# Optimization experiments

Hardware: AMD Instinct MI355X
Metric: run time of the kernel (lower is better)

## Reference

```python
import jax, jax.numpy as jnp
import numpy as np

LN_EPS = 1e-5

def _layer_norm(x, g, b):
    mu = jnp.mean(x, axis=-1, keepdims=True)
    var = jnp.mean(jnp.square(x - mu), axis=-1, keepdims=True)
    return g * (x - mu) * jax.lax.rsqrt(var + LN_EPS) + b

def setup_inputs() -> dict:
    key = jax.random.key(0)
    ks = jax.random.split(key, 12)
    N, E, D, V = 25000, 400000, 128, 16
    x = jax.random.normal(ks[0], (N, 3), dtype=jnp.float32)
    h = jax.random.normal(ks[1], (N, D), dtype=jnp.float32)
    edge_index = jax.random.randint(ks[2], (2, E), 0, N, dtype=jnp.int64)
    local_frames = jax.random.normal(ks[3], (N, 3, 3), dtype=jnp.float32)
    batch = jnp.zeros((N,), dtype=jnp.int64)
    v_prev = jax.random.normal(ks[4], (N, V, 3), dtype=jnp.float32)
    # vector_init params: Linear(D, 3V) -> LN -> SiLU -> Linear(3V, 3V) -> LN -> SiLU
    lim1 = np.sqrt(6.0 / (D + 3 * V))
    W1 = jax.random.uniform(ks[5], (3 * V, D), minval=-lim1, maxval=lim1, dtype=jnp.float32)
    b1 = jnp.zeros((3 * V,), jnp.float32)
    g1 = jnp.ones((3 * V,), jnp.float32); bb1 = jnp.zeros((3 * V,), jnp.float32)
    lim2 = np.sqrt(6.0 / (3 * V + 3 * V))
    W2 = jax.random.uniform(ks[6], (3 * V, 3 * V), minval=-lim2, maxval=lim2, dtype=jnp.float32)
    b2 = jnp.zeros((3 * V,), jnp.float32)
    g2 = jnp.ones((3 * V,), jnp.float32); bb2 = jnp.zeros((3 * V,), jnp.float32)
    # vector_interaction params: Linear(2D, 2V*V) -> LN -> Sigmoid
    limi = np.sqrt(6.0 / (2 * D + 2 * V * V))
    Wi = jax.random.uniform(ks[7], (2 * V * V, 2 * D), minval=-limi, maxval=limi, dtype=jnp.float32)
    bi = jnp.zeros((2 * V * V,), jnp.float32)
    gi = jnp.ones((2 * V * V,), jnp.float32); bbi = jnp.zeros((2 * V * V,), jnp.float32)
    return {"x": x, "h": h, "edge_index": edge_index, "local_frames": local_frames,
            "batch": batch, "v_prev": v_prev,
            "W1": W1, "b1": b1, "g1": g1, "bb1": bb1,
            "W2": W2, "b2": b2, "g2": g2, "bb2": bb2,
            "Wi": Wi, "bi": bi, "gi": gi, "bbi": bbi}

def reference(x, h, edge_index, local_frames, batch, v_prev,
              W1, b1, g1, bb1, W2, b2, g2, bb2, Wi, bi, gi, bbi):
    N = x.shape[0]
    V = v_prev.shape[1]  # vector_dim
    row, col = edge_index[0], edge_index[1]
    # vector_init: two Linear+LN+SiLU blocks -> [N, V, 3]
    t = jax.nn.silu(_layer_norm(h @ W1.T + b1, g1, bb1))
    t = jax.nn.silu(_layer_norm(t @ W2.T + b2, g2, bb2))
    vectors = t.reshape(N, V, 3)
    hi, hj = h[col], h[row]           # [E, D]
    vi, vj = vectors[col], vectors[row]  # [E, V, 3]
    Ri, Rj = local_frames[col], local_frames[row]  # [E, 3, 3]
    # R_rel = Ri^T @ Rj
    R_rel = jnp.einsum('eji,ejk->eik', Ri, Rj)
    vj_in_i = jnp.einsum('eij,ecj->eci', R_rel, vj)  # rotate sender vectors
    stacked_vectors = jnp.concatenate([vi, vj_in_i], axis=1)  # [E, 2V, 3]
    stacked_norms = jnp.concatenate([hi, hj], axis=-1)        # [E, 2D]
    w = jax.nn.sigmoid(_layer_norm(stacked_norms @ Wi.T + bi, gi, bbi))
    int_weights = w.reshape(-1, 2 * V, V)                     # [E, 2V, V]
    v_new = jnp.einsum('eko,ekc->eco', stacked_vectors, int_weights)  # [E, V, 3]
    v_out = jax.ops.segment_sum(v_new, col, num_segments=N)  # scatter-add on receiver
    return v_prev + v_out
```

## Files before the change

kernel.cpp:

```cpp
#include <hip/hip_runtime.h>


#define DD 128
#define VV 16
#define TV 48
#define NK 512

__device__ __forceinline__ float bf2f_hi(unsigned u){
    union{unsigned u; float f;} v; v.u = u & 0xffff0000u; return v.f;
}
__device__ __forceinline__ float bf2f_lo(unsigned u){
    union{unsigned u; float f;} v; v.u = u << 16; return v.f;
}
__device__ __forceinline__ unsigned short f2bf(float f){
    union{float f; unsigned u;} v; v.f = f;
    unsigned r = v.u + 0x7fffu + ((v.u >> 16) & 1u);
    return (unsigned short)(r >> 16);
}
__device__ __forceinline__ void unpack8(uint4 q, float* d){
    d[0]=bf2f_lo(q.x); d[1]=bf2f_hi(q.x);
    d[2]=bf2f_lo(q.y); d[3]=bf2f_hi(q.y);
    d[4]=bf2f_lo(q.z); d[5]=bf2f_hi(q.z);
    d[6]=bf2f_lo(q.w); d[7]=bf2f_hi(q.w);
}
__device__ __forceinline__ float waveRedSum64(float v){
    #pragma unroll
    for (int off = 32; off > 0; off >>= 1) v += __shfl_xor(v, off, 64);
    return v;
}

__global__ void detect_i64(const int* p, int nchk, int* flag){
    __shared__ int s;
    if (threadIdx.x == 0) s = 0;
    __syncthreads();
    int nz = 0;
    for (int i = threadIdx.x; i < nchk; i += blockDim.x) nz |= (p[2*i+1] != 0);
    if (nz) atomicOr(&s, 1);
    __syncthreads();
    if (threadIdx.x == 0) *flag = s ? 0 : 1;
}

__global__ void zero_cnt(int* cnt, int n){
    int i = blockIdx.x*blockDim.x + threadIdx.x;
    if (i < n) cnt[i] = 0;
}

__global__ void cvt_hist(const void* __restrict__ src, int* __restrict__ dst,
                         int* __restrict__ cnt, int n, int E,
                         const int* __restrict__ flag){
    int i = blockIdx.x*blockDim.x + threadIdx.x;
    if (i >= n) return;
    int v = (*flag) ? (int)((const long long*)src)[i] : ((const int*)src)[i];
    dst[i] = v;
    if (i >= E) atomicAdd(&cnt[v], 1);
}

__global__ __launch_bounds__(1024) void scan_k(const int* __restrict__ cnt,
        int* __restrict__ start, int* __restrict__ cursor, int N){
    __shared__ int wsum[16];
    __shared__ int woff[16];
    __shared__ int btot;
    __shared__ int carry;
    int tid = threadIdx.x;
    int lane = tid & 63, wid = tid >> 6;
    if (tid == 0) carry = 0;
    __syncthreads();
    for (int base = 0; base < N; base += 1024){
        int i = base + tid;
        int x = (i < N) ? cnt[i] : 0;
        int v = x;
        #pragma unroll
        for (int off = 1; off < 64; off <<= 1){
            int t = __shfl_up(v, off, 64);
            if (lane >= off) v += t;
        }
        if (lane == 63) wsum[wid] = v;
        __syncthreads();
        if (wid == 0 && lane < 16){
            int s = wsum[lane];
            int sv = s;
            #pragma unroll
            for (int off = 1; off < 16; off <<= 1){
                int t = __shfl_up(sv, off, 64);
                if (lane >= off) sv += t;
            }
            woff[lane] = sv - s;
            if (lane == 15) btot = sv;
        }
        __syncthreads();
        if (i < N){
            int excl = v - x + woff[wid] + carry;
            start[i] = excl;
            cursor[i] = excl;
        }
        __syncthreads();
        if (tid == 0) carry += btot;
        __syncthreads();
    }
    if (tid == 0) start[N] = carry;
}

__global__ void scatter_k(const int* __restrict__ idx, int* __restrict__ cursor,
                          int* __restrict__ elist, int E){
    int e = blockIdx.x*blockDim.x + threadIdx.x;
    if (e >= E) return;
    int col = idx[E + e], row = idx[e];
    int pos = atomicAdd(&cursor[col], 1);
    elist[pos] = row;
}

__global__ void build_wt(const float* __restrict__ Wi, const float* __restrict__ bi,
                         const float* __restrict__ gi, const float* __restrict__ bbi,
                         float* __restrict__ Wt, float* __restrict__ bias_t,
                         float* __restrict__ gi_t, float* __restrict__ bbi_t){
    int j = blockIdx.x;
    int d = threadIdx.x;
    int half = j >> 9;
    int jj = j & 511;
    int c = jj >> 5, kk = jj & 31;
    int k = kk*16 + c;
    Wt[d*1024 + j] = Wi[k*256 + half*128 + d];
    if (d == 0){
        bias_t[j] = half ? 0.0f : bi[k];
        if (!half){ gi_t[jj] = gi[k]; bbi_t[jj] = bbi[k]; }
    }
}

__global__ __launch_bounds__(256) void vinit(
        const float* __restrict__ h,
        const float* __restrict__ W1, const float* __restrict__ b1,
        const float* __restrict__ g1, const float* __restrict__ bb1,
        const float* __restrict__ W2, const float* __restrict__ b2,
        const float* __restrict__ g2, const float* __restrict__ bb2,
        const float* __restrict__ frames,
        float* __restrict__ vecs, float* __restrict__ gvec, int N){
    __shared__ float hs[4][DD];
    __shared__ float ts[4][TV];
    int w = threadIdx.x >> 6, l = threadIdx.x & 63;
    int n = blockIdx.x*4 + w;
    int nr = n < N ? n : N-1;
    hs[w][l]      = h[(size_t)nr*DD + l];
    hs[w][l + 64] = h[(size_t)nr*DD + 64 + l];
    __syncthreads();

    float o1 = 0.0f;
    if (l < TV){
        o1 = b1[l];
        const float* wr = W1 + l*DD;
        #pragma unroll
        for (int d = 0; d < DD; d += 4){
            float4 w4 = *(const float4*)(wr + d);
            o1 += hs[w][d]*w4.x + hs[w][d+1]*w4.y + hs[w][d+2]*w4.z + hs[w][d+3]*w4.w;
        }
    }
    float s  = waveRedSum64(l < TV ? o1 : 0.0f);
    float mu = s * (1.0f/TV);
    float dv = l < TV ? (o1 - mu) : 0.0f;
    float sq = waveRedSum64(dv*dv);
    float inv = rsqrtf(sq*(1.0f/TV) + 1e-5f);
    if (l < TV){
        float y = g1[l]*(dv*inv) + bb1[l];
        ts[w][l] = y / (1.0f + __expf(-y));
    }
    __syncthreads();

    float o2 = 0.0f;
    if (l < TV){
        o2 = b2[l];
        const float* wr = W2 + l*TV;
        #pragma unroll
        for (int j = 0; j < TV; j += 4){
            float4 w4 = *(const float4*)(wr + j);
            o2 += ts[w][j]*w4.x + ts[w][j+1]*w4.y + ts[w][j+2]*w4.z + ts[w][j+3]*w4.w;
        }
    }
    s  = waveRedSum64(l < TV ? o2 : 0.0f);
    mu = s * (1.0f/TV);
    dv = l < TV ? (o2 - mu) : 0.0f;
    sq = waveRedSum64(dv*dv);
    inv = rsqrtf(sq*(1.0f/TV) + 1e-5f);
    __syncthreads();
    if (l < TV){
        float y = g2[l]*(dv*inv) + bb2[l];
        float t2 = y / (1.0f + __expf(-y));
        if (n < N) vecs[(size_t)n*TV + l] = t2;
        ts[w][l] = t2;
    }
    __syncthreads();
    if (l < TV && n < N){
        int cc = l/3, oo = l%3;
        const float* R = frames + (size_t)n*9;
        float gv = R[oo*3+0]*ts[w][cc*3+0] + R[oo*3+1]*ts[w][cc*3+1] + R[oo*3+2]*ts[w][cc*3+2];
        gvec[(size_t)n*TV + l] = gv;
    }
}

#define BM 64
#define BN 128
#define BK 32
__global__ __launch_bounds__(256) void gemm_p(
        const float* __restrict__ h, const float* __restrict__ Wt,
        const float* __restrict__ bias_t, unsigned short* __restrict__ P, int N){
    __shared__ float As[BK][BM];
    __shared__ float Bs[BK][BN + 4];
    int tid = threadIdx.x;
    int n0 = blockIdx.x * BN;
    int m0 = blockIdx.y * BM;
    int tm = tid >> 4, tn = tid & 15;
    float acc[4][8];
    #pragma unroll
    for (int i = 0; i < 4; i++)
        #pragma unroll
        for (int j = 0; j < 8; j++) acc[i][j] = 0.0f;

    int lm  = tid >> 2;
    int lc4 = tid & 3;
    int grow = m0 + lm; if (grow > N-1) grow = N-1;
    const float* hp = h + (size_t)grow*DD + lc4*8;
    int bkb = tid >> 5;
    int bjj = tid & 31;

    for (int kt = 0; kt < DD; kt += BK){
        float4 a0 = *(const float4*)(hp + kt);
        float4 a1 = *(const float4*)(hp + kt + 4);
        As[lc4*8+0][lm] = a0.x; As[lc4*8+1][lm] = a0.y;
        As[lc4*8+2][lm] = a0.z; As[lc4*8+3][lm] = a0.w;
        As[lc4*8+4][lm] = a1.x; As[lc4*8+5][lm] = a1.y;
        As[lc4*8+6][lm] = a1.z; As[lc4*8+7][lm] = a1.w;
        #pragma unroll
        for (int r = 0; r < 4; r++){
            float4 b4 = *(const float4*)(Wt + (size_t)(kt + bkb*4 + r)*1024 + n0 + bjj*4);
            *(float4*)&Bs[bkb*4+r][bjj*4] = b4;
        }
        __syncthreads();
        #pragma unroll
        for (int k = 0; k < BK; k++){
            float4 a   = *(const float4*)&As[k][tm*4];
            float4 blo = *(const float4*)&Bs[k][tn*4];
            float4 bhi = *(const float4*)&Bs[k][64 + tn*4];
            float am[4] = {a.x, a.y, a.z, a.w};
            float bv[8] = {blo.x, blo.y, blo.z, blo.w, bhi.x, bhi.y, bhi.z, bhi.w};
            #pragma unroll
            for (int mi = 0; mi < 4; mi++)
                #pragma unroll
                for (int ni = 0; ni < 8; ni++)
                    acc[mi][ni] = fmaf(am[mi], bv[ni], acc[mi][ni]);
        }
        __syncthreads();
    }
    #pragma unroll
    for (int mi = 0; mi < 4; mi++){
        size_t rowm = (size_t)(m0 + tm*4 + mi);
        ushort4 olo, ohi;
        olo.x = f2bf(acc[mi][0] + bias_t[n0 + tn*4 + 0]);
        olo.y = f2bf(acc[mi][1] + bias_t[n0 + tn*4 + 1]);
        olo.z = f2bf(acc[mi][2] + bias_t[n0 + tn*4 + 2]);
        olo.w = f2bf(acc[mi][3] + bias_t[n0 + tn*4 + 3]);
        ohi.x = f2bf(acc[mi][4] + bias_t[n0 + 64 + tn*4 + 0]);
        ohi.y = f2bf(acc[mi][5] + bias_t[n0 + 64 + tn*4 + 1]);
        ohi.z = f2bf(acc[mi][6] + bias_t[n0 + 64 + tn*4 + 2]);
        ohi.w = f2bf(acc[mi][7] + bias_t[n0 + 64 + tn*4 + 3]);
        *(ushort4*)(P + rowm*1024 + n0 + tn*4)      = olo;
        *(ushort4*)(P + rowm*1024 + n0 + 64 + tn*4) = ohi;
    }
}

__global__ __launch_bounds__(256) void node_k(
        const unsigned short* __restrict__ P,
        const float* __restrict__ vecs, const float* __restrict__ gvec,
        const float* __restrict__ frames, const int* __restrict__ start,
        const int* __restrict__ elist, const float* __restrict__ vprev,
        const float* __restrict__ gi_t, const float* __restrict__ bbi_t,
        float* __restrict__ out, int N){
    __shared__ float vi_s[4][TV];
    __shared__ float vj_s[4][4][52];
    int wv = threadIdx.x >> 6, ln = threadIdx.x & 63;
    int sub = ln >> 4, c = ln & 15;
    int n0 = blockIdx.x*4 + wv;
    int n = n0 < N ? n0 : N-1;

    if (ln < TV) vi_s[wv][ln] = vecs[(size_t)n*TV + ln];
    float R[9];
    #pragma unroll
    for (int i = 0; i < 9; i++) R[i] = frames[(size_t)n*9 + i];

    float pa[32];
    {
        const uint4* p4 = (const uint4*)(P + (size_t)n*1024 + c*32);
        #pragma unroll
        for (int q = 0; q < 4; q++) unpack8(p4[q], pa + 8*q);
    }
    int e0 = start[n], e1 = start[n+1];
    float a0 = 0.f, a1 = 0.f, a2 = 0.f;

    for (int t = e0 + sub; t < e1; t += 4){
        int row = elist[t];
        float l[32]; float s = 0.f;
        {
            const uint4* p4 = (const uint4*)(P + (size_t)row*1024 + 512 + c*32);
            #pragma unroll
            for (int q = 0; q < 4; q++){
                float tmp[8]; unpack8(p4[q], tmp);
                #pragma unroll
                for (int r = 0; r < 8; r++){
                    float x = pa[8*q+r] + tmp[r];
                    l[8*q+r] = x; s += x;
                }
            }
        }
        #pragma unroll
        for (int off = 1; off < 16; off <<= 1) s += __shfl_xor(s, off, 64);
        float mu = s * (1.0f/NK);
        float sq = 0.f;
        #pragma unroll
        for (int i = 0; i < 32; i++){ float d = l[i] - mu; l[i] = d; sq = fmaf(d, d, sq); }
        #pragma unroll
        for (int off = 1; off < 16; off <<= 1) sq += __shfl_xor(sq, off, 64);
        float inv = rsqrtf(sq*(1.0f/NK) + 1e-5f);

        float w[32];
        {
            const float4* g4 = (const float4*)(gi_t  + c*32);
            const float4* b4 = (const float4*)(bbi_t + c*32);
            #pragma unroll
            for (int q = 0; q < 8; q++){
                float4 gg = g4[q], bb = b4[q];
                float gx[4] = {gg.x, gg.y, gg.z, gg.w};
                float bx[4] = {bb.x, bb.y, bb.z, bb.w};
                #pragma unroll
                for (int r = 0; r < 4; r++){
                    float y = fmaf(gx[r], l[4*q+r]*inv, bx[r]);
                    w[4*q+r] = 1.0f / (1.0f + __expf(-y));
                }
            }
        }
        {
            const float* gr = gvec + (size_t)row*TV + c*3;
            float g0 = gr[0], g1 = gr[1], g2 = gr[2];
            #pragma unroll
            for (int i = 0; i < 3; i++)
                vj_s[wv][sub][c*3+i] = R[0+i]*g0 + R[3+i]*g1 + R[6+i]*g2;
        }
        #pragma unroll
        for (int kk = 0; kk < 16; kk++){
            float wl = w[kk], wh = w[16+kk];
            a0 = fmaf(vi_s[wv][kk*3+0], wl, a0);
            a1 = fmaf(vi_s[wv][kk*3+1], wl, a1);
            a2 = fmaf(vi_s[wv][kk*3+2], wl, a2);
            a0 = fmaf(vj_s[wv][sub][kk*3+0], wh, a0);
            a1 = fmaf(vj_s[wv][sub][kk*3+1], wh, a1);
            a2 = fmaf(vj_s[wv][sub][kk*3+2], wh, a2);
        }
    }
    a0 += __shfl_xor(a0,16,64); a0 += __shfl_xor(a0,32,64);
    a1 += __shfl_xor(a1,16,64); a1 += __shfl_xor(a1,32,64);
    a2 += __shfl_xor(a2,16,64); a2 += __shfl_xor(a2,32,64);
    if (ln < 16 && n0 < N){
        size_t o = (size_t)n*TV + c*3;
        out[o+0] = vprev[o+0] + a0;
        out[o+1] = vprev[o+1] + a1;
        out[o+2] = vprev[o+2] + a2;
    }
}

extern "C" void kernel_launch(void* const* d_in, const int* in_sizes, int n_in,
                              void* d_out, int out_size, void* d_ws, size_t ws_size,
                              hipStream_t stream){
    const float* h      = (const float*)d_in[1];
    const void*  eidx   = d_in[2];
    const float* frames = (const float*)d_in[3];
    const float* vprev  = (const float*)d_in[5];
    const float* W1  = (const float*)d_in[6];
    const float* b1  = (const float*)d_in[7];
    const float* g1  = (const float*)d_in[8];
    const float* bb1 = (const float*)d_in[9];
    const float* W2  = (const float*)d_in[10];
    const float* b2  = (const float*)d_in[11];
    const float* g2  = (const float*)d_in[12];
    const float* bb2 = (const float*)d_in[13];
    const float* Wi  = (const float*)d_in[14];
    const float* bi  = (const float*)d_in[15];
    const float* gi  = (const float*)d_in[16];
    const float* bbi = (const float*)d_in[17];
    float* out = (float*)d_out;

    const int N = in_sizes[1] / DD;
    const int E = in_sizes[2] / 2;
    const int Np = ((N + 63) / 64) * 64;

    float* ws     = (float*)d_ws;
    float* Wt     = ws;
    float* bias_t = Wt + 131072;
    float* gi_t   = bias_t + 1024;
    float* bbi_t  = gi_t + 512;
    float* vecs   = bbi_t + 512;
    float* gvec   = vecs + (size_t)N*TV;
    unsigned short* P = (unsigned short*)(gvec + (size_t)N*TV);
    int*   idx32  = (int*)(P + (size_t)Np*1024);
    int*   cnt    = idx32 + 2*(size_t)E;
    int*   startp = cnt + N;
    int*   cursor = startp + N + 1;
    int*   elist  = cursor + N;
    int*   dflag  = elist + E;

    int nchk = E < 4096 ? E : 4096;
    detect_i64<<<1, 256, 0, stream>>>((const int*)eidx, nchk, dflag);
    zero_cnt<<<(N + 255)/256, 256, 0, stream>>>(cnt, N);
    cvt_hist<<<(2*E + 255)/256, 256, 0, stream>>>(eidx, idx32, cnt, 2*E, E, dflag);
    build_wt<<<1024, 128, 0, stream>>>(Wi, bi, gi, bbi, Wt, bias_t, gi_t, bbi_t);
    vinit<<<(N + 3)/4, 256, 0, stream>>>(h, W1, b1, g1, bb1, W2, b2, g2, bb2,
                                         frames, vecs, gvec, N);
    dim3 ggrid(1024/BN, Np/BM);
    gemm_p<<<ggrid, 256, 0, stream>>>(h, Wt, bias_t, P, N);
    scan_k<<<1, 1024, 0, stream>>>(cnt, startp, cursor, N);
    scatter_k<<<(E + 255)/256, 256, 0, stream>>>(idx32, cursor, elist, E);
    node_k<<<(N + 3)/4, 256, 0, stream>>>(P, vecs, gvec, frames, startp, elist,
                                          vprev, gi_t, bbi_t, out, N);
    (void)ws_size; (void)n_in; (void)out_size;
}
```

Measured before the change: 590.8 us.

## Use bf16 MFMA with hi/lo split for projection GEMM, store fp32 P

Replaces the scalar FP32 tiled GEMM with an MFMA bf16 kernel. The h operand is split into high and low bf16 parts to keep accuracy, while the weights are cast to bf16. The intermediate P is now stored as fp32 rather than bf16, which doubles gather traffic in node_k. node_k also switches to a single-pass mean/variance LayerNorm, folds the sign into gi/bbi, and precomputes rotated sender vectors into a shared buffer. This trades extra memory bandwidth in the edge loop for a much cheaper GEMM and less ALU work per edge.

```diff
diff --git a/kernel.cpp b/kernel.cpp
--- a/kernel.cpp
+++ b/kernel.cpp
@@ -6,27 +6,16 @@
 #define TV 48
 #define NK 512
 
-__device__ __forceinline__ float bf2f_hi(unsigned u){
-    union{unsigned u; float f;} v; v.u = u & 0xffff0000u; return v.f;
-}
-__device__ __forceinline__ float bf2f_lo(unsigned u){
-    union{unsigned u; float f;} v; v.u = u << 16; return v.f;
-}
+typedef __attribute__((ext_vector_type(8))) short short8;
+typedef __attribute__((ext_vector_type(4))) float f32x4;
+
 __device__ __forceinline__ unsigned short f2bf(float f){
     union{float f; unsigned u;} v; v.f = f;
     unsigned r = v.u + 0x7fffu + ((v.u >> 16) & 1u);
     return (unsigned short)(r >> 16);
 }
-__device__ __forceinline__ void unpack8(uint4 q, float* d){
-    d[0]=bf2f_lo(q.x); d[1]=bf2f_hi(q.x);
-    d[2]=bf2f_lo(q.y); d[3]=bf2f_hi(q.y);
-    d[4]=bf2f_lo(q.z); d[5]=bf2f_hi(q.z);
-    d[6]=bf2f_lo(q.w); d[7]=bf2f_hi(q.w);
-}
-__device__ __forceinline__ float waveRedSum64(float v){
-    #pragma unroll
-    for (int off = 32; off > 0; off >>= 1) v += __shfl_xor(v, off, 64);
-    return v;
+__device__ __forceinline__ float bf2f(unsigned short h){
+    union{unsigned u; float f;} v; v.u = ((unsigned)h) << 16; return v.f;
 }
 
 __global__ void detect_i64(const int* p, int nchk, int* flag){
@@ -111,7 +100,7 @@
 
 __global__ void build_wt(const float* __restrict__ Wi, const float* __restrict__ bi,
                          const float* __restrict__ gi, const float* __restrict__ bbi,
-                         float* __restrict__ Wt, float* __restrict__ bias_t,
+                         unsigned short* __restrict__ Wtb, float* __restrict__ bias_t,
                          float* __restrict__ gi_t, float* __restrict__ bbi_t){
     int j = blockIdx.x;
     int d = threadIdx.x;
@@ -119,13 +108,30 @@
     int jj = j & 511;
     int c = jj >> 5, kk = jj & 31;
     int k = kk*16 + c;
-    Wt[d*1024 + j] = Wi[k*256 + half*128 + d];
+    Wtb[(size_t)j*128 + d] = f2bf(Wi[k*256 + half*128 + d]);
     if (d == 0){
         bias_t[j] = half ? 0.0f : bi[k];
-        if (!half){ gi_t[jj] = gi[k]; bbi_t[jj] = bbi[k]; }
-    }
-}
-
+        if (!half){ gi_t[jj] = -gi[k]; bbi_t[jj] = -bbi[k]; }
+    }
+}
+
+__global__ void cast_h(const float* __restrict__ h, unsigned short* __restrict__ hbh,
+                       unsigned short* __restrict__ hbl, int N, int total){
+    int i = blockIdx.x*blockDim.x + threadIdx.x;
+    if (i >= total) return;
+    int m = i >> 7;
+    float v = (m < N) ? h[i] : 0.0f;
+    unsigned short hi = f2bf(v);
+    float lo = v - bf2f(hi);
+    hbh[i] = hi;
+    hbl[i] = f2bf(lo);
+}
+
+__device__ __forceinline__ float waveRedSum64(float v){
+    #pragma unroll
+    for (int off = 32; off > 0; off >>= 1) v += __shfl_xor(v, off, 64);
+    return v;
+}
 __global__ __launch_bounds__(256) void vinit(
         const float* __restrict__ h,
         const float* __restrict__ W1, const float* __restrict__ b1,
@@ -195,130 +201,118 @@
     }
 }
 
-#define BM 64
-#define BN 128
-#define BK 32
-__global__ __launch_bounds__(256) void gemm_p(
-        const float* __restrict__ h, const float* __restrict__ Wt,
-        const float* __restrict__ bias_t, unsigned short* __restrict__ P, int N){
-    __shared__ float As[BK][BM];
-    __shared__ float Bs[BK][BN + 4];
-    int tid = threadIdx.x;
-    int n0 = blockIdx.x * BN;
-    int m0 = blockIdx.y * BM;
-    int tm = tid >> 4, tn = tid & 15;
-    float acc[4][8];
+__global__ __launch_bounds__(256) void gemm_mfma(
+        const unsigned short* __restrict__ hbh, const unsigned short* __restrict__ hbl,
+        const unsigned short* __restrict__ Wtb, const float* __restrict__ bias_t,
+        float* __restrict__ P, int Np){
+    int wv = threadIdx.x >> 6, l = threadIdx.x & 63;
+    int lr = l & 15, g = l >> 4;
+    int m0 = (blockIdx.y*4 + wv)*16;
+    int n0 = blockIdx.x*256;
+
+    f32x4 acc[16];
     #pragma unroll
-    for (int i = 0; i < 4; i++)
-        #pragma unroll
-        for (int j = 0; j < 8; j++) acc[i][j] = 0.0f;
-
-    int lm  = tid >> 2;
-    int lc4 = tid & 3;
-    int grow = m0 + lm; if (grow > N-1) grow = N-1;
-    const float* hp = h + (size_t)grow*DD + lc4*8;
-    int bkb = tid >> 5;
-    int bjj = tid & 31;
-
-    for (int kt = 0; kt < DD; kt += BK){
-        float4 a0 = *(const float4*)(hp + kt);
-        float4 a1 = *(const float4*)(hp + kt + 4);
-        As[lc4*8+0][lm] = a0.x; As[lc4*8+1][lm] = a0.y;
-        As[lc4*8+2][lm] = a0.z; As[lc4*8+3][lm] = a0.w;
-        As[lc4*8+4][lm] = a1.x; As[lc4*8+5][lm] = a1.y;
-        As[lc4*8+6][lm] = a1.z; As[lc4*8+7][lm] = a1.w;
+    for (int nf = 0; nf < 16; nf++) acc[nf] = (f32x4){0.f,0.f,0.f,0.f};
+
+    const unsigned short* arow_h = hbh + (size_t)(m0 + lr)*128;
+    const unsigned short* arow_l = hbl + (size_t)(m0 + lr)*128;
+
+    #pragma unroll
+    for (int ks = 0; ks < 128; ks += 32){
+        int kb = ks + 4*g;
+        short8 ah, al;
+        ((ushort4*)&ah)[0] = *(const ushort4*)(arow_h + kb);
+        ((ushort4*)&ah)[1] = *(const ushort4*)(arow_h + kb + 16);
+        ((ushort4*)&al)[0] = *(const ushort4*)(arow_l + kb);
+        ((ushort4*)&al)[1] = *(const ushort4*)(arow_l + kb + 16);
+        #pragma unroll
+        for (int nf = 0; nf < 16; nf++){
+            const unsigned short* brow = Wtb + (size_t)(n0 + nf*16 + lr)*128;
+            short8 b;
+            ((ushort4*)&b)[0] = *(const ushort4*)(brow + kb);
+            ((ushort4*)&b)[1] = *(const ushort4*)(brow + kb + 16);
+            acc[nf] = __builtin_amdgcn_mfma_f32_16x16x32_bf16(ah, b, acc[nf], 0, 0, 0);
+            acc[nf] = __builtin_amdgcn_mfma_f32_16x16x32_bf16(al, b, acc[nf], 0, 0, 0);
+        }
+    }
+    #pragma unroll
+    for (int nf = 0; nf < 16; nf++){
+        int col = n0 + nf*16 + lr;
+        float bs = bias_t[col];
         #pragma unroll
         for (int r = 0; r < 4; r++){
-            float4 b4 = *(const float4*)(Wt + (size_t)(kt + bkb*4 + r)*1024 + n0 + bjj*4);
-            *(float4*)&Bs[bkb*4+r][bjj*4] = b4;
-        }
-        __syncthreads();
-        #pragma unroll
-        for (int k = 0; k < BK; k++){
-            float4 a   = *(const float4*)&As[k][tm*4];
-            float4 blo = *(const float4*)&Bs[k][tn*4];
-            float4 bhi = *(const float4*)&Bs[k][64 + tn*4];
-            float am[4] = {a.x, a.y, a.z, a.w};
-            float bv[8] = {blo.x, blo.y, blo.z, blo.w, bhi.x, bhi.y, bhi.z, bhi.w};
-            #pragma unroll
-            for (int mi = 0; mi < 4; mi++)
-                #pragma unroll
-                for (int ni = 0; ni < 8; ni++)
-                    acc[mi][ni] = fmaf(am[mi], bv[ni], acc[mi][ni]);
-        }
-        __syncthreads();
-    }
-    #pragma unroll
-    for (int mi = 0; mi < 4; mi++){
-        size_t rowm = (size_t)(m0 + tm*4 + mi);
-        ushort4 olo, ohi;
-        olo.x = f2bf(acc[mi][0] + bias_t[n0 + tn*4 + 0]);
-        olo.y = f2bf(acc[mi][1] + bias_t[n0 + tn*4 + 1]);
-        olo.z = f2bf(acc[mi][2] + bias_t[n0 + tn*4 + 2]);
-        olo.w = f2bf(acc[mi][3] + bias_t[n0 + tn*4 + 3]);
-        ohi.x = f2bf(acc[mi][4] + bias_t[n0 + 64 + tn*4 + 0]);
-        ohi.y = f2bf(acc[mi][5] + bias_t[n0 + 64 + tn*4 + 1]);
-        ohi.z = f2bf(acc[mi][6] + bias_t[n0 + 64 + tn*4 + 2]);
-        ohi.w = f2bf(acc[mi][7] + bias_t[n0 + 64 + tn*4 + 3]);
-        *(ushort4*)(P + rowm*1024 + n0 + tn*4)      = olo;
-        *(ushort4*)(P + rowm*1024 + n0 + 64 + tn*4) = ohi;
+            P[(size_t)(m0 + g*4 + r)*1024 + col] = acc[nf][r] + bs;
+        }
     }
 }
 
 __global__ __launch_bounds__(256) void node_k(
-        const unsigned short* __restrict__ P,
-        const float* __restrict__ vecs, const float* __restrict__ gvec,
-        const float* __restrict__ frames, const int* __restrict__ start,
-        const int* __restrict__ elist, const float* __restrict__ vprev,
-        const float* __restrict__ gi_t, const float* __restrict__ bbi_t,
-        float* __restrict__ out, int N){
-    __shared__ float vi_s[4][TV];
-    __shared__ float vj_s[4][4][52];
+        const float* __restrict__ P, const float* __restrict__ vecs,
+        const float* __restrict__ gvec, const float* __restrict__ frames,
+        const int* __restrict__ start, const int* __restrict__ elist,
+        const float* __restrict__ vprev, const float* __restrict__ gi_t,
+        const float* __restrict__ bbi_t, float* __restrict__ out, int N){
+    __shared__ float svs[4][4][100];
     int wv = threadIdx.x >> 6, ln = threadIdx.x & 63;
     int sub = ln >> 4, c = ln & 15;
     int n0 = blockIdx.x*4 + wv;
     int n = n0 < N ? n0 : N-1;
 
-    if (ln < TV) vi_s[wv][ln] = vecs[(size_t)n*TV + ln];
+    {
+        const float* vc = vecs + (size_t)n*TV + c*3;
+        svs[wv][sub][c*3+0] = vc[0];
+        svs[wv][sub][c*3+1] = vc[1];
+        svs[wv][sub][c*3+2] = vc[2];
+    }
     float R[9];
     #pragma unroll
     for (int i = 0; i < 9; i++) R[i] = frames[(size_t)n*9 + i];
 
     float pa[32];
     {
-        const uint4* p4 = (const uint4*)(P + (size_t)n*1024 + c*32);
-        #pragma unroll
-        for (int q = 0; q < 4; q++) unpack8(p4[q], pa + 8*q);
+        const float4* p4 = (const float4*)(P + (size_t)n*1024 + c*32);
+        #pragma unroll
+        for (int q = 0; q < 8; q++){
+            float4 t = p4[q];
+            pa[4*q+0]=t.x; pa[4*q+1]=t.y; pa[4*q+2]=t.z; pa[4*q+3]=t.w;
+        }
     }
     int e0 = start[n], e1 = start[n+1];
     float a0 = 0.f, a1 = 0.f, a2 = 0.f;
 
     for (int t = e0 + sub; t < e1; t += 4){
         int row = elist[t];
-        float l[32]; float s = 0.f;
+        float l[32]; float s = 0.f, s2 = 0.f;
         {
-            const uint4* p4 = (const uint4*)(P + (size_t)row*1024 + 512 + c*32);
+            const float4* p4 = (const float4*)(P + (size_t)row*1024 + 512 + c*32);
             #pragma unroll
-            for (int q = 0; q < 4; q++){
-                float tmp[8]; unpack8(p4[q], tmp);
-                #pragma unroll
-                for (int r = 0; r < 8; r++){
-                    float x = pa[8*q+r] + tmp[r];
-                    l[8*q+r] = x; s += x;
-                }
+            for (int q = 0; q < 8; q++){
+                float4 b = p4[q];
+                float t0 = pa[4*q+0]+b.x, t1 = pa[4*q+1]+b.y;
+                float t2v = pa[4*q+2]+b.z, t3 = pa[4*q+3]+b.w;
+                l[4*q+0]=t0; l[4*q+1]=t1; l[4*q+2]=t2v; l[4*q+3]=t3;
+                s += t0; s2 = fmaf(t0,t0,s2);
+                s += t1; s2 = fmaf(t1,t1,s2);
+                s += t2v; s2 = fmaf(t2v,t2v,s2);
+                s += t3; s2 = fmaf(t3,t3,s2);
             }
         }
         #pragma unroll
-        for (int off = 1; off < 16; off <<= 1) s += __shfl_xor(s, off, 64);
-        float mu = s * (1.0f/NK);
-        float sq = 0.f;
-        #pragma unroll
-        for (int i = 0; i < 32; i++){ float d = l[i] - mu; l[i] = d; sq = fmaf(d, d, sq); }
-        #pragma unroll
-        for (int off = 1; off < 16; off <<= 1) sq += __shfl_xor(sq, off, 64);
-        float inv = rsqrtf(sq*(1.0f/NK) + 1e-5f);
-
-        float w[32];
+        for (int off = 1; off < 16; off <<= 1){
+            s  += __shfl_xor(s,  off, 64);
+            s2 += __shfl_xor(s2, off, 64);
+        }
+        float mu  = s * (1.0f/NK);
+        float var = fmaf(-mu, mu, s2 * (1.0f/NK));
+        float inv = rsqrtf(var + 1e-5f);
+
+        {
+            const float* gr = gvec + (size_t)row*TV + c*3;
+            float g0 = gr[0], g1 = gr[1], g2 = gr[2];
+            svs[wv][sub][48+c*3+0] = R[0]*g0 + R[3]*g1 + R[6]*g2;
+            svs[wv][sub][48+c*3+1] = R[1]*g0 + R[4]*g1 + R[7]*g2;
+            svs[wv][sub][48+c*3+2] = R[2]*g0 + R[5]*g1 + R[8]*g2;
+        }
         {
             const float4* g4 = (const float4*)(gi_t  + c*32);
             const float4* b4 = (const float4*)(bbi_t + c*32);
@@ -329,27 +323,30 @@
                 float bx[4] = {bb.x, bb.y, bb.z, bb.w};
                 #pragma unroll
                 for (int r = 0; r < 4; r++){
-                    float y = fmaf(gx[r], l[4*q+r]*inv, bx[r]);
-                    w[4*q+r] = 1.0f / (1.0f + __expf(-y));
+                    float z = (l[4*q+r] - mu) * inv;
+                    float yn = fmaf(gx[r], z, bx[r]);
+                    l[4*q+r] = 1.0f / (1.0f + __expf(yn));
                 }
             }
         }
         {
-            const float* gr = gvec + (size_t)row*TV + c*3;
-            float g0 = gr[0], g1 = gr[1], g2 = gr[2];
+            const float4* sv4 = (const float4*)&svs[wv][sub][0];
             #pragma unroll
-            for (int i = 0; i < 3; i++)
-                vj_s[wv][sub][c*3+i] = R[0+i]*g0 + R[3+i]*g1 + R[6+i]*g2;
-        }
-        #pragma unroll
-        for (int kk = 0; kk < 16; kk++){
-            float wl = w[kk], wh = w[16+kk];
-            a0 = fmaf(vi_s[wv][kk*3+0], wl, a0);
-            a1 = fmaf(vi_s[wv][kk*3+1], wl, a1);
-            a2 = fmaf(vi_s[wv][kk*3+2], wl, a2);
-            a0 = fmaf(vj_s[wv][sub][kk*3+0], wh, a0);
-            a1 = fmaf(vj_s[wv][sub][kk*3+1], wh, a1);
-            a2 = fmaf(vj_s[wv][sub][kk*3+2], wh, a2);
+            for (int q = 0; q < 24; q++){
+                float4 x = sv4[q];
+                {   const int e = 4*q+0, ch = e/3, o = e%3;
+                    float p = x.x * l[ch];
+                    if (o==0) a0 += p; else if (o==1) a1 += p; else a2 += p; }
+                {   const int e = 4*q+1, ch = e/3, o = e%3;
+                    float p = x.y * l[ch];
+                    if (o==0) a0 += p; else if (o==1) a1 += p; else a2 += p; }
+                {   const int e = 4*q+2, ch = e/3, o = e%3;
+                    float p = x.z * l[ch];
+                    if (o==0) a0 += p; else if (o==1) a1 += p; else a2 += p; }
+                {   const int e = 4*q+3, ch = e/3, o = e%3;
+                    float p = x.w * l[ch];
+                    if (o==0) a0 += p; else if (o==1) a1 += p; else a2 += p; }
+            }
         }
     }
     a0 += __shfl_xor(a0,16,64); a0 += __shfl_xor(a0,32,64);
@@ -388,30 +385,33 @@
     const int E = in_sizes[2] / 2;
     const int Np = ((N + 63) / 64) * 64;
 
-    float* ws     = (float*)d_ws;
-    float* Wt     = ws;
-    float* bias_t = Wt + 131072;
+    float* bias_t = (float*)d_ws;
     float* gi_t   = bias_t + 1024;
     float* bbi_t  = gi_t + 512;
     float* vecs   = bbi_t + 512;
     float* gvec   = vecs + (size_t)N*TV;
-    unsigned short* P = (unsigned short*)(gvec + (size_t)N*TV);
-    int*   idx32  = (int*)(P + (size_t)Np*1024);
-    int*   cnt    = idx32 + 2*(size_t)E;
-    int*   startp = cnt + N;
-    int*   cursor = startp + N + 1;
-    int*   elist  = cursor + N;
-    int*   dflag  = elist + E;
+    unsigned short* Wtb = (unsigned short*)(gvec + (size_t)N*TV);
+    unsigned short* hbh = Wtb + 1024*128;
+    unsigned short* hbl = hbh + (size_t)Np*128;
+    int* idx32  = (int*)(hbl + (size_t)Np*128);
+    int* cnt    = idx32 + 2*(size_t)E;
+    int* startp = cnt + N;
+    int* cursor = startp + N + 1;
+    int* elist  = cursor + N;
+    int* dflag  = elist + E;
+    uintptr_t pb = (uintptr_t)(dflag + 1);
+    pb = (pb + 15) & ~(uintptr_t)15;
+    float* P = (float*)pb;
 
     int nchk = E < 4096 ? E : 4096;
     detect_i64<<<1, 256, 0, stream>>>((const int*)eidx, nchk, dflag);
     zero_cnt<<<(N + 255)/256, 256, 0, stream>>>(cnt, N);
     cvt_hist<<<(2*E + 255)/256, 256, 0, stream>>>(eidx, idx32, cnt, 2*E, E, dflag);
-    build_wt<<<1024, 128, 0, stream>>>(Wi, bi, gi, bbi, Wt, bias_t, gi_t, bbi_t);
+    build_wt<<<1024, 128, 0, stream>>>(Wi, bi, gi, bbi, Wtb, bias_t, gi_t, bbi_t);
+    cast_h<<<(Np*DD + 255)/256, 256, 0, stream>>>(h, hbh, hbl, N, Np*DD);
     vinit<<<(N + 3)/4, 256, 0, stream>>>(h, W1, b1, g1, bb1, W2, b2, g2, bb2,
                                          frames, vecs, gvec, N);
-    dim3 ggrid(1024/BN, Np/BM);
-    gemm_p<<<ggrid, 256, 0, stream>>>(h, Wt, bias_t, P, N);
+    gemm_mfma<<<dim3(4, Np/64), 256, 0, stream>>>(hbh, hbl, Wtb, bias_t, P, Np);
     scan_k<<<1, 1024, 0, stream>>>(cnt, startp, cursor, N);
     scatter_k<<<(E + 255)/256, 256, 0, stream>>>(idx32, cursor, elist, E);
     node_k<<<(N + 3)/4, 256, 0, stream>>>(P, vecs, gvec, frames, startp, elist,
```

After: 732.2 us. +23.9%, slower.
